# Performance work log

Hardware: AMD Instinct MI355X
Metric: run time of the kernel (lower is better)

Reference implementation:

```python
import jax, jax.numpy as jnp
import numpy as np
import math

ALPHA = 0.5


def _dfrft_matrix(N: int, a: float) -> np.ndarray:
    """Candan's discrete fractional Fourier transform matrix (approx order 2),
    as used by torch-frft's dfrft. D(a) = E diag(exp(-i*pi/2*a*k)) E^T, where E
    are eigenvectors (even/odd interleaved, descending eigenvalue) of the
    S = circulant([0,1,0,...,0,1]) + diag(Re fft(s)) matrix that commutes with the DFT.
    Pure numpy; runs at trace time (constants)."""
    s = np.zeros(N)
    s[1] = 1.0
    s[-1] = 1.0
    idx = (np.arange(N)[:, None] - np.arange(N)[None, :]) % N
    S = s[idx] + np.diag(np.fft.fft(s).real)
    # odd/even decomposition matrix P (orthogonal)
    r = N // 2
    even = 1 - (N % 2)
    P = np.zeros((N, N))
    P[0, 0] = 1.0
    c = 1.0 / math.sqrt(2.0)
    for i in range(1, r - even + 1):
        P[i, i] = c
        P[i, N - i] = c
    if even:
        P[r, r] = 1.0
    for i in range(r + 1, N):
        P[i, i] = -c
        P[i, N - i] = c
    CS = P @ S @ P.T
    C2 = CS[: r + 1, : r + 1]
    S2 = CS[r + 1:, r + 1:]
    _, vc = np.linalg.eigh(C2)  # ascending -> reverse for descending order
    _, vs = np.linalg.eigh(S2)
    SC2 = (P @ np.vstack((vc, np.zeros((N - r - 1, r + 1)))))[:, ::-1]  # even evecs
    SS2 = (P @ np.vstack((np.zeros((r + 1, N - r - 1)), vs)))[:, ::-1]  # odd evecs
    if N % 2 == 0:
        E = np.zeros((N, N + 1))
        E[:, 0::2] = SC2
        E[:, 1::2] = np.hstack((SS2, np.zeros((N, 1))))
        E = np.delete(E, N - 1, axis=1)  # skip eigenvalue index N-1, keep N
    else:
        E = np.zeros((N, N))
        E[:, 0::2] = SC2
        E[:, 1::2] = SS2
    shift = 1 - (N % 2)
    k = np.concatenate((np.arange(N - 1), [N - 1 + shift]))
    f = np.exp(-1j * (np.pi / 2.0) * a * k)
    return (E * f[None, :]) @ E.T


def setup_inputs() -> dict:
    key = jax.random.key(0)
    k1, k2, k3, k4, k5 = jax.random.split(key, 5)
    B, Ci, Co, H, W = 16, 64, 64, 128, 128
    scale = 1.0 / Ci
    return {
        "x": jax.random.normal(k1, (B, Ci, H, W), jnp.float32),
        "w_r": jax.random.normal(k2, (Co, Ci), jnp.float32) * scale,
        "w_i": jax.random.normal(k3, (Co, Ci), jnp.float32) * scale,
        "b_r": jax.random.normal(k4, (Co,), jnp.float32) * scale,
        "b_i": jax.random.normal(k5, (Co,), jnp.float32) * scale,
    }


def reference(x, w_r, w_i, b_r, b_i):
    B, Ci, H, W = x.shape
    Aw = jnp.asarray(_dfrft_matrix(W, ALPHA), jnp.complex64)   # dfrft along dim=-1
    Ah = jnp.asarray(_dfrft_matrix(H, ALPHA), jnp.complex64)   # dfrft along dim=-2
    xc = x.astype(jnp.complex64)
    # forward fractional Fourier transforms
    x_ft = jnp.einsum('wv,bchv->bchw', Aw, xc)
    x_ft = jnp.einsum('hg,bcgw->bchw', Ah, x_ft)
    # 1x1 complex conv (complex weight + bias)
    wc = w_r.astype(jnp.complex64) + 1j * w_i.astype(jnp.complex64)
    bc = b_r.astype(jnp.complex64) + 1j * b_i.astype(jnp.complex64)
    out_ft = jnp.einsum('oi,bihw->bohw', wc, x_ft) + bc[None, :, None, None]
    # inverse transforms: D(-a) = conj(D(a)) since eigenvectors are real
    y = jnp.einsum('hg,bogw->bohw', jnp.conj(Ah), out_ft)
    y = jnp.einsum('wv,bohv->bohw', jnp.conj(Aw), y)
    # module returns a complex tensor; expose as stacked (real, imag)
    return jnp.stack((y.real, y.imag), axis=0)
```

## Files before the change

kernel.cpp:

```cpp
#include <hip/hip_runtime.h>
#include <cmath>
#include <cstring>
#include <vector>
#include <algorithm>


struct UV { float ur[128]; float ui[128]; };
static UV g_uv;

namespace {

constexpr int NN = 128;

void matmul_d(const std::vector<double>& A, const std::vector<double>& B,
              std::vector<double>& C, int n) {
  for (int i = 0; i < n; ++i)
    for (int j = 0; j < n; ++j) {
      double s = 0.0;
      for (int k = 0; k < n; ++k) s += A[(size_t)i*n+k] * B[(size_t)k*n+j];
      C[(size_t)i*n+j] = s;
    }
}

void jacobi_eigh(std::vector<double>& A, int n, std::vector<double>& V,
                 std::vector<double>& lam) {
  V.assign((size_t)n*n, 0.0);
  for (int i = 0; i < n; ++i) V[(size_t)i*n+i] = 1.0;
  for (int sweep = 0; sweep < 200; ++sweep) {
    double off = 0.0;
    for (int p = 0; p < n; ++p)
      for (int q = p+1; q < n; ++q) off += A[(size_t)p*n+q]*A[(size_t)p*n+q];
    if (off < 1e-24) break;
    for (int p = 0; p < n-1; ++p)
      for (int q = p+1; q < n; ++q) {
        double apq = A[(size_t)p*n+q];
        if (std::fabs(apq) < 1e-300) continue;
        double app = A[(size_t)p*n+p], aqq = A[(size_t)q*n+q];
        double tau = (aqq - app) / (2.0*apq);
        double t = (tau >= 0 ? 1.0 : -1.0) / (std::fabs(tau) + std::sqrt(1.0 + tau*tau));
        double c = 1.0/std::sqrt(1.0 + t*t), s = t*c;
        for (int k = 0; k < n; ++k) {
          double akp = A[(size_t)k*n+p], akq = A[(size_t)k*n+q];
          A[(size_t)k*n+p] = c*akp - s*akq;
          A[(size_t)k*n+q] = s*akp + c*akq;
        }
        for (int k = 0; k < n; ++k) {
          double apk = A[(size_t)p*n+k], aqk = A[(size_t)q*n+k];
          A[(size_t)p*n+k] = c*apk - s*aqk;
          A[(size_t)q*n+k] = s*apk + c*aqk;
        }
        for (int k = 0; k < n; ++k) {
          double vkp = V[(size_t)k*n+p], vkq = V[(size_t)k*n+q];
          V[(size_t)k*n+p] = c*vkp - s*vkq;
          V[(size_t)k*n+q] = s*vkp + c*vkq;
        }
      }
  }
  lam.resize(n);
  for (int i = 0; i < n; ++i) lam[i] = A[(size_t)i*n+i];
}

bool init_uv() {
  const int n = NN, r = NN/2;
  const double c = 1.0/std::sqrt(2.0);
  const double PI = 3.14159265358979323846;
  std::vector<double> S((size_t)n*n, 0.0), P((size_t)n*n, 0.0);
  for (int i = 0; i < n; ++i) {
    S[(size_t)i*n+i] = 2.0*std::cos(2.0*PI*i/n);
    S[(size_t)i*n + (i+1)%n] += 1.0;
    S[(size_t)i*n + (i-1+n)%n] += 1.0;
  }
  P[0] = 1.0;
  for (int i = 1; i <= r-1; ++i) { P[(size_t)i*n+i] = c;  P[(size_t)i*n + (n-i)] = c; }
  P[(size_t)r*n+r] = 1.0;
  for (int i = r+1; i < n; ++i)  { P[(size_t)i*n+i] = -c; P[(size_t)i*n + (n-i)] = c; }
  std::vector<double> Pt((size_t)n*n), T((size_t)n*n), CS((size_t)n*n);
  for (int i = 0; i < n; ++i)
    for (int j = 0; j < n; ++j) Pt[(size_t)i*n+j] = P[(size_t)j*n+i];
  matmul_d(P, S, T, n);
  matmul_d(T, Pt, CS, n);
  const int m = r + 1;
  std::vector<double> C2((size_t)m*m);
  for (int i = 0; i < m; ++i)
    for (int j = 0; j < m; ++j) C2[(size_t)i*m+j] = CS[(size_t)i*n+j];
  std::vector<double> V, lam;
  jacobi_eigh(C2, m, V, lam);
  std::vector<int> idx(m);
  for (int i = 0; i < m; ++i) idx[i] = i;
  std::sort(idx.begin(), idx.end(), [&](int a, int b){ return lam[a] < lam[b]; });
  double ure[NN] = {0}, uim[NN] = {0};
  for (int mm = 0; mm < m; ++mm) {
    int col = idx[m-1-mm];
    double q[NN];
    q[0] = V[(size_t)0*m+col];
    for (int j = 1; j <= r-1; ++j) q[j] = c * V[(size_t)j*m+col];
    q[r] = V[(size_t)r*m+col];
    for (int j = r+1; j < n; ++j)  q[j] = c * V[(size_t)(n-j)*m+col];
    double ssum = 0.0;
    for (int j = 0; j < n; ++j) ssum += q[j];
    switch (mm & 3) {
      case 0: for (int h = 0; h < n; ++h) ure[h] += q[h]*ssum; break;
      case 1: for (int h = 0; h < n; ++h) uim[h] += q[h]*ssum; break;
      case 2: for (int h = 0; h < n; ++h) ure[h] -= q[h]*ssum; break;
      case 3: for (int h = 0; h < n; ++h) uim[h] -= q[h]*ssum; break;
    }
  }
  for (int h = 0; h < n; ++h) { g_uv.ur[h] = (float)ure[h]; g_uv.ui[h] = (float)uim[h]; }
  return true;
}

bool g_inited = init_uv();

}


__global__ __launch_bounds__(256) void transpose_w_kernel(
    const float* __restrict__ wr, const float* __restrict__ wi,
    float* __restrict__ wTr, float* __restrict__ wTi) {
  int t = blockIdx.x * 256 + threadIdx.x;
  if (t < 4096) {
    int o = t >> 6, i = t & 63;
    wTr[i*64 + o] = wr[t];
    wTi[i*64 + o] = wi[t];
  }
}

__global__ __launch_bounds__(512, 8) void spec_main_kernel(
    const float* __restrict__ x,
    const float* __restrict__ wTr, const float* __restrict__ wTi,
    const float* __restrict__ br, const float* __restrict__ bi,
    float* __restrict__ out, UV uv) {
  const int tid  = threadIdx.x;
  const int bid  = blockIdx.x;
  const int b    = bid >> 7;
  const int hrow = bid & 127;
  const int lane = tid & 63;
  const int o0   = __builtin_amdgcn_readfirstlane((tid >> 6) << 3);
  const int w0   = lane << 1;
  const long long pos0 = (long long)hrow << 7;
  const float* xp = x + ((long long)b << 20) + pos0 + w0;

  const float uhr = uv.ur[hrow], uhi = uv.ui[hrow];
  const float v0r = uv.ur[w0],   v0i = uv.ui[w0];
  const float v1r = uv.ur[w0+1], v1i = uv.ui[w0+1];
  const float g0r = uhr*v0r - uhi*v0i, g0i = uhr*v0i + uhi*v0r;
  const float g1r = uhr*v1r - uhi*v1i, g1i = uhr*v1i + uhi*v1r;

  float accr[8][2], acci[8][2];
#pragma unroll
  for (int oo = 0; oo < 8; ++oo) {
    float bro = br[o0+oo], bio = bi[o0+oo];
    accr[oo][0] = bro*g0r - bio*g0i;  acci[oo][0] = bro*g0i + bio*g0r;
    accr[oo][1] = bro*g1r - bio*g1i;  acci[oo][1] = bro*g1i + bio*g1r;
  }

  float2 c0 = *(const float2*)(xp);
  float2 c1 = *(const float2*)(xp + 16384);
#pragma unroll 1
  for (int i = 0; i < 64; i += 2) {
    const int p0 = (i + 2 < 64) ? i + 2 : 63;
    const int p1 = (i + 3 < 64) ? i + 3 : 63;
    float2 n0 = *(const float2*)(xp + ((long long)p0 << 14));
    float2 n1 = *(const float2*)(xp + ((long long)p1 << 14));
    const float* wr0 = wTr + (i << 6) + o0;
    const float* wi0 = wTi + (i << 6) + o0;
#pragma unroll
    for (int oo = 0; oo < 8; ++oo) {
      float wr = wr0[oo], wi = wi0[oo];
      accr[oo][0] += wr*c0.x;  accr[oo][1] += wr*c0.y;
      acci[oo][0] += wi*c0.x;  acci[oo][1] += wi*c0.y;
    }
#pragma unroll
    for (int oo = 0; oo < 8; ++oo) {
      float wr = wr0[64+oo], wi = wi0[64+oo];
      accr[oo][0] += wr*c1.x;  accr[oo][1] += wr*c1.y;
      acci[oo][0] += wi*c1.x;  acci[oo][1] += wi*c1.y;
    }
    c0 = n0; c1 = n1;
  }

  long long baseR = (((long long)(b*64 + o0)) << 14) + pos0 + w0;
  long long baseI = baseR + ((long long)(16*64) << 14);
#pragma unroll
  for (int oo = 0; oo < 8; ++oo) {
    *(float2*)&out[baseR + ((long long)oo << 14)] = make_float2(accr[oo][0], accr[oo][1]);
    *(float2*)&out[baseI + ((long long)oo << 14)] = make_float2(acci[oo][0], acci[oo][1]);
  }
}

extern "C" void kernel_launch(void* const* d_in, const int* in_sizes, int n_in,
                              void* d_out, int out_size, void* d_ws, size_t ws_size,
                              hipStream_t stream) {
  (void)in_sizes; (void)n_in; (void)out_size; (void)ws_size; (void)g_inited;
  const float* x  = (const float*)d_in[0];
  const float* wr = (const float*)d_in[1];
  const float* wi = (const float*)d_in[2];
  const float* br = (const float*)d_in[3];
  const float* bi = (const float*)d_in[4];
  float* out = (float*)d_out;
  float* wTr = (float*)d_ws;
  float* wTi = wTr + 4096;

  transpose_w_kernel<<<16, 256, 0, stream>>>(wr, wi, wTr, wTi);
  spec_main_kernel<<<2048, 512, 0, stream>>>(x, wTr, wTi, br, bi, out, g_uv);
}
```

Measured before the change: 225.5 us.

## Stage input channels in LDS via async global-to-LDS loads, two rows per block

Each block now handles two H rows and copies all 64 input channels for those rows into a 64KB shared buffer using global_load_lds. The copy is split into two halves so the second half loads while the first is being used. Before this, each of the 8 waves re-read the same x values from global memory. Each thread now computes 4 consecutive positions and writes float4 outputs, with half as many blocks and a lower launch-bounds occupancy hint. The large LDS footprint limits how many blocks fit per CU, and correctness relies on the barriers also waiting for the asynchronous LDS loads.

Measured after the change: 209.6 us. 1.08x faster.

```diff
diff --git a/kernel.cpp b/kernel.cpp
--- a/kernel.cpp
+++ b/kernel.cpp
@@ -114,6 +114,9 @@
 }
 
 
+typedef const float __attribute__((address_space(1)))* gas_fp;
+typedef float __attribute__((address_space(3)))* las_fp;
+
 __global__ __launch_bounds__(256) void transpose_w_kernel(
     const float* __restrict__ wr, const float* __restrict__ wi,
     float* __restrict__ wTr, float* __restrict__ wTi) {
@@ -125,66 +128,101 @@
   }
 }
 
-__global__ __launch_bounds__(512, 8) void spec_main_kernel(
+__global__ __launch_bounds__(512, 4) void spec_main_kernel(
     const float* __restrict__ x,
     const float* __restrict__ wTr, const float* __restrict__ wTi,
     const float* __restrict__ br, const float* __restrict__ bi,
     float* __restrict__ out, UV uv) {
+  __shared__ float xs[64][256];
   const int tid  = threadIdx.x;
   const int bid  = blockIdx.x;
-  const int b    = bid >> 7;
-  const int hrow = bid & 127;
+  const int b    = bid >> 6;
+  const int pair = bid & 63;
+  const int wave = tid >> 6;
   const int lane = tid & 63;
-  const int o0   = __builtin_amdgcn_readfirstlane((tid >> 6) << 3);
-  const int w0   = lane << 1;
-  const long long pos0 = (long long)hrow << 7;
-  const float* xp = x + ((long long)b << 20) + pos0 + w0;
+  const int row  = lane >> 5;
+  const int p4   = (lane & 31) << 2;
+  const int o0   = __builtin_amdgcn_readfirstlane(wave << 3);
+  const int hrow = (pair << 1) + row;
+  const int loff = (row << 7) + p4;
+
+  const float* xb = x + ((long long)b << 20) + ((long long)hrow << 7) + p4;
+
+#pragma unroll
+  for (int j = 0; j < 4; ++j) {
+    int c = (wave << 2) + j;
+    __builtin_amdgcn_global_load_lds((gas_fp)(xb + ((long long)c << 14)),
+                                     (las_fp)&xs[c][0], 16, 0, 0);
+  }
+  __syncthreads();
+
+#pragma unroll
+  for (int j = 0; j < 4; ++j) {
+    int c = 32 + (wave << 2) + j;
+    __builtin_amdgcn_global_load_lds((gas_fp)(xb + ((long long)c << 14)),
+                                     (las_fp)&xs[c][0], 16, 0, 0);
+  }
 
   const float uhr = uv.ur[hrow], uhi = uv.ui[hrow];
-  const float v0r = uv.ur[w0],   v0i = uv.ui[w0];
-  const float v1r = uv.ur[w0+1], v1i = uv.ui[w0+1];
-  const float g0r = uhr*v0r - uhi*v0i, g0i = uhr*v0i + uhi*v0r;
-  const float g1r = uhr*v1r - uhi*v1i, g1i = uhr*v1i + uhi*v1r;
-
-  float accr[8][2], acci[8][2];
+  float gr[4], gi[4];
+#pragma unroll
+  for (int k = 0; k < 4; ++k) {
+    float vr = uv.ur[p4+k], vi = uv.ui[p4+k];
+    gr[k] = uhr*vr - uhi*vi;
+    gi[k] = uhr*vi + uhi*vr;
+  }
+
+  float accr[8][4], acci[8][4];
 #pragma unroll
   for (int oo = 0; oo < 8; ++oo) {
     float bro = br[o0+oo], bio = bi[o0+oo];
-    accr[oo][0] = bro*g0r - bio*g0i;  acci[oo][0] = bro*g0i + bio*g0r;
-    accr[oo][1] = bro*g1r - bio*g1i;  acci[oo][1] = bro*g1i + bio*g1r;
-  }
-
-  float2 c0 = *(const float2*)(xp);
-  float2 c1 = *(const float2*)(xp + 16384);
-#pragma unroll 1
-  for (int i = 0; i < 64; i += 2) {
-    const int p0 = (i + 2 < 64) ? i + 2 : 63;
-    const int p1 = (i + 3 < 64) ? i + 3 : 63;
-    float2 n0 = *(const float2*)(xp + ((long long)p0 << 14));
-    float2 n1 = *(const float2*)(xp + ((long long)p1 << 14));
+#pragma unroll
+    for (int k = 0; k < 4; ++k) {
+      accr[oo][k] = bro*gr[k] - bio*gi[k];
+      acci[oo][k] = bro*gi[k] + bio*gr[k];
+    }
+  }
+
+#pragma unroll 4
+  for (int i = 0; i < 32; ++i) {
+    float4 xv = *(const float4*)&xs[i][loff];
     const float* wr0 = wTr + (i << 6) + o0;
     const float* wi0 = wTi + (i << 6) + o0;
 #pragma unroll
     for (int oo = 0; oo < 8; ++oo) {
       float wr = wr0[oo], wi = wi0[oo];
-      accr[oo][0] += wr*c0.x;  accr[oo][1] += wr*c0.y;
-      acci[oo][0] += wi*c0.x;  acci[oo][1] += wi*c0.y;
-    }
+      accr[oo][0] += wr*xv.x;  accr[oo][1] += wr*xv.y;
+      accr[oo][2] += wr*xv.z;  accr[oo][3] += wr*xv.w;
+      acci[oo][0] += wi*xv.x;  acci[oo][1] += wi*xv.y;
+      acci[oo][2] += wi*xv.z;  acci[oo][3] += wi*xv.w;
+    }
+  }
+  __syncthreads();
+
+#pragma unroll 4
+  for (int i = 32; i < 64; ++i) {
+    float4 xv = *(const float4*)&xs[i][loff];
+    const float* wr0 = wTr + (i << 6) + o0;
+    const float* wi0 = wTi + (i << 6) + o0;
 #pragma unroll
     for (int oo = 0; oo < 8; ++oo) {
-      float wr = wr0[64+oo], wi = wi0[64+oo];
-      accr[oo][0] += wr*c1.x;  accr[oo][1] += wr*c1.y;
-      acci[oo][0] += wi*c1.x;  acci[oo][1] += wi*c1.y;
-    }
-    c0 = n0; c1 = n1;
-  }
-
-  long long baseR = (((long long)(b*64 + o0)) << 14) + pos0 + w0;
+      float wr = wr0[oo], wi = wi0[oo];
+      accr[oo][0] += wr*xv.x;  accr[oo][1] += wr*xv.y;
+      accr[oo][2] += wr*xv.z;  accr[oo][3] += wr*xv.w;
+      acci[oo][0] += wi*xv.x;  acci[oo][1] += wi*xv.y;
+      acci[oo][2] += wi*xv.z;  acci[oo][3] += wi*xv.w;
+    }
+  }
+
+  const long long posg  = ((long long)hrow << 7) + p4;
+  long long baseR = ((long long)(b*64 + o0) << 14) + posg;
   long long baseI = baseR + ((long long)(16*64) << 14);
 #pragma unroll
   for (int oo = 0; oo < 8; ++oo) {
-    *(float2*)&out[baseR + ((long long)oo << 14)] = make_float2(accr[oo][0], accr[oo][1]);
-    *(float2*)&out[baseI + ((long long)oo << 14)] = make_float2(acci[oo][0], acci[oo][1]);
+    *(float4*)&out[baseR + ((long long)oo << 14)] =
+        make_float4(accr[oo][0], accr[oo][1], accr[oo][2], accr[oo][3]);
+    *(float4*)&out[baseI + ((long long)oo << 14)] =
+        make_float4(acci[oo][0], acci[oo][1], acci[oo][2], acci[oo][3]);
   }
 }
 
@@ -202,5 +240,5 @@
   float* wTi = wTr + 4096;
 
   transpose_w_kernel<<<16, 256, 0, stream>>>(wr, wi, wTr, wTi);
-  spec_main_kernel<<<2048, 512, 0, stream>>>(x, wTr, wTi, br, bi, out, g_uv);
-}
+  spec_main_kernel<<<1024, 512, 0, stream>>>(x, wTr, wTi, br, bi, out, g_uv);
+}
```
